# Performance work log

Hardware: AMD Instinct MI355X
Metric: run time of the kernel (lower is better)

Reference implementation:

```python
import jax, jax.numpy as jnp
import numpy as np

B, T, DIN, D = 8, 2048, 1024, 1024
EPS = 1e-6


def setup_inputs() -> dict:
    key = jax.random.key(0)
    k0, k1, k2, k3 = jax.random.split(key, 4)
    x = jax.random.normal(k0, (B, T, DIN), dtype=jnp.float32)
    h0 = jax.random.normal(k1, (B, D), dtype=jnp.float32)
    s0 = jax.random.normal(k2, (B, D), dtype=jnp.float32)
    # xavier_uniform for weight [7D, DIN]
    bound = float(np.sqrt(6.0 / (DIN + 7 * D)))
    W = jax.random.uniform(k3, (7 * D, DIN), dtype=jnp.float32, minval=-bound, maxval=bound)
    # structured bias init from _init_weights: [0, 1, 0, 0, 0, 2, 0.5] per block
    b = jnp.concatenate([
        jnp.zeros(D), jnp.ones(D), jnp.zeros(D), jnp.zeros(D),
        jnp.zeros(D), jnp.full((D,), 2.0), jnp.full((D,), 0.5)
    ]).astype(jnp.float32)
    return {"x": x, "h0": h0, "s0": s0, "W": W, "b": b}


def _forward(x, h0, s0, W, b):
    Bv, Tv, _ = x.shape
    Dv = W.shape[0] // 7
    gates = (jnp.einsum('bti,oi->bto', x, W) + b).reshape(Bv, Tv, 7, Dv)
    r, z, k, v, h_pre, decay, alpha = (gates[:, :, i] for i in range(7))
    # per-element pairwise RMS norms, exactly as in the Triton kernel
    rms_control = jnp.sqrt((r * r + z * z) / 2 + EPS)
    rms_kv = jnp.sqrt((k * k + v * v) / 2 + EPS)
    # r is normalized+sigmoided in the kernel but never used -> no effect on output
    z = jax.nn.sigmoid(z / rms_control)
    decay = jax.nn.sigmoid(decay / jnp.sqrt(decay * decay + EPS))
    alpha = jax.nn.sigmoid(alpha / jnp.sqrt(alpha * alpha + EPS))
    h_pre = h_pre / jnp.sqrt(h_pre * h_pre + EPS)
    kv = (k / rms_kv) * (v / rms_kv) / (rms_kv * rms_kv + EPS)
    # time-major [T,B,D] for the scan
    seq = tuple(jnp.swapaxes(a, 0, 1) for a in (z, kv, h_pre, decay, alpha))

    def step(carry, ins):
        h, s = carry
        z_t, kv_t, hp_t, d_t, a_t = ins
        s = d_t * s + a_t * kv_t
        c = jax.nn.sigmoid(2.0 * (hp_t + s)) * 2.0 - 1.0
        h = (1.0 - z_t) * c + z_t * h
        return (h, s), h

    (_, sT), out = jax.lax.scan(step, (h0, s0), seq)
    return jnp.swapaxes(out, 0, 1), sT  # ([B,T,D], [B,D])


def reference(x, h0, s0, W, b):
    return _forward(x, h0, s0, W, b)
```

## Files before the change

kernel.cpp:

```cpp
#include <hip/hip_runtime.h>
#include <hip/hip_bf16.h>

typedef _Float16 f16x8 __attribute__((ext_vector_type(8)));
typedef float f32x4 __attribute__((ext_vector_type(4)));

static constexpr int BB = 8;
static constexpr int TT = 2048;
static constexpr int DD = 1024;
static constexpr int MM = BB * TT;
static constexpr int NN = 7 * DD;
static constexpr int KP = 3072;
static constexpr int NCSUB = 32;
static constexpr int LC = TT / NCSUB;
static constexpr int BD = BB * DD;
#define EPS_ 1e-6f

static constexpr size_t SZ_CMP = (size_t)MM * DD * 8;
static constexpr size_t SZ_BP  = (size_t)NN * KP * 2;
static constexpr size_t SZ_SM  = (size_t)NCSUB * BD * 4;
static constexpr size_t OFF_BP  = SZ_CMP;
static constexpr size_t OFF_SM  = OFF_BP + SZ_BP;
static constexpr size_t OFF_AP  = OFF_SM + 6 * SZ_SM;
static constexpr size_t CHUNK_BYTES = (size_t)MM * KP * 2 + (size_t)MM * NN * 2;

__device__ __forceinline__ unsigned short bf_rne(float f) {
    unsigned u = __builtin_bit_cast(unsigned, f);
    unsigned r = (u + 0x7fffu + ((u >> 16) & 1u)) >> 16;
    return (unsigned short)r;
}
__device__ __forceinline__ float bf2f(unsigned short u) {
    return __builtin_bit_cast(float, ((unsigned)u) << 16);
}
__device__ __forceinline__ float f16f(unsigned short u) {
    return (float)__builtin_bit_cast(_Float16, u);
}
__device__ __forceinline__ unsigned short f16b(float f) {
    return __builtin_bit_cast(unsigned short, (_Float16)f);
}
__device__ __forceinline__ float sigm(float x) { return 1.0f / (1.0f + __expf(-x)); }

typedef __attribute__((address_space(3))) void lds_void;
typedef const __attribute__((address_space(1))) void gbl_void;
__device__ __forceinline__ void gload16(const void* g, void* l) {
    __builtin_amdgcn_global_load_lds((gbl_void*)g, (lds_void*)l, 16, 0, 0);
}

__global__ __launch_bounds__(256) void prep_w(const float* __restrict__ W,
                                              _Float16* __restrict__ Bp1,
                                              _Float16* __restrict__ Bp2) {
    int i = blockIdx.x * 256 + threadIdx.x;
    int o = i >> 10, k = i & 1023;
    int g = o >> 10, d = o & 1023;
    float wv = W[i] * 512.0f;
    _Float16 w1 = (_Float16)wv;
    _Float16 w2 = (_Float16)(wv - (float)w1);
    if (g == 0 || g == 1 || g == 4) {
        int r1 = (g == 4 ? 2 : g) * 1024 + d;
        Bp1[(size_t)r1 * 1024 + k] = w1;
    } else {
        int r2 = (g < 4 ? g - 2 : g - 3) * 1024 + d;
        size_t base = (size_t)r2 * 3072 + k;
        Bp2[base] = w1; Bp2[base + 1024] = w1; Bp2[base + 2048] = w2;
    }
}

__global__ __launch_bounds__(256) void prep_x(const float* __restrict__ x,
                                              _Float16* __restrict__ Ap,
                                              int tc, int Tc, int tcShift) {
    int i = blockIdx.x * 256 + threadIdx.x;
    int rho = i >> 10, k = i & 1023;
    int b = rho >> tcShift, tau = rho & (Tc - 1);
    size_t m = (size_t)b * TT + (size_t)tc * Tc + tau;
    float xv = x[m * DD + k] * 16.0f;
    _Float16 x1 = (_Float16)xv;
    _Float16 x2 = (_Float16)(xv - (float)x1);
    size_t base = (size_t)rho * KP + k;
    Ap[base] = x1; Ap[base + 1024] = x2; Ap[base + 2048] = x1;
}

template<int KT, int NTILES, int NCOLS, int KIND>
__global__ __launch_bounds__(512) void gemm_k(const _Float16* __restrict__ Ap,
                                              const _Float16* __restrict__ Bp,
                                              const float* __restrict__ bias,
                                              _Float16* __restrict__ Gc, int Mt) {
    constexpr int KSTR = KT * 64;
    __shared__ __align__(16) _Float16 As[256 * 64];
    __shared__ __align__(16) _Float16 Bs[128 * 64];
    int nwg = Mt * NTILES;
    int bid = blockIdx.x;
    int cpx = nwg >> 3;
    int swz = (bid & 7) * cpx + (bid >> 3);
    int bm = swz / NTILES, bn = swz % NTILES;
    int m0 = bm * 256, n0 = bn * 128;
    int tid = threadIdx.x;
    int w = tid >> 6, l = tid & 63;
    int wm = w >> 1, wn = w & 1;
    int lrow = l & 15, kg = l >> 4;
    f32x4 acc[4][4] = {};
    const char* Ab = (const char*)Ap;
    const char* Bb = (const char*)Bp;
    for (int k0 = 0; k0 < KT * 64; k0 += 64) {
#pragma unroll
        for (int q = 0; q < 4; ++q) {
            int c = q * 512 + tid;
            int row = c >> 3, sgg = (c & 7) ^ (row & 7);
            gload16(Ab + ((size_t)(m0 + row) * KP + k0 + sgg * 8) * 2, (char*)As + c * 16);
        }
#pragma unroll
        for (int q = 0; q < 2; ++q) {
            int c = q * 512 + tid;
            int row = c >> 3, sgg = (c & 7) ^ (row & 7);
            gload16(Bb + ((size_t)(n0 + row) * KSTR + k0 + sgg * 8) * 2, (char*)Bs + c * 16);
        }
        __syncthreads();
#pragma unroll
        for (int kk = 0; kk < 64; kk += 32) {
            f16x8 af[4], bfr[4];
            int sgb = kg + (kk >> 3);
#pragma unroll
            for (int i = 0; i < 4; ++i) {
                int r = wm * 64 + i * 16 + lrow;
                af[i] = *(const f16x8*)(As + r * 64 + (size_t)((sgb ^ (r & 7)) * 8));
            }
#pragma unroll
            for (int j = 0; j < 4; ++j) {
                int r = wn * 64 + j * 16 + lrow;
                bfr[j] = *(const f16x8*)(Bs + r * 64 + (size_t)((sgb ^ (r & 7)) * 8));
            }
#pragma unroll
            for (int i = 0; i < 4; ++i)
#pragma unroll
                for (int j = 0; j < 4; ++j)
                    acc[i][j] = __builtin_amdgcn_mfma_f32_16x16x32_f16(af[i], bfr[j], acc[i][j], 0, 0, 0);
        }
        __syncthreads();
    }
    const float inv = 1.0f / 8192.0f;
#pragma unroll
    for (int j = 0; j < 4; ++j) {
        int o = n0 + wn * 64 + j * 16 + lrow;
        int g = o >> 10, d = o & 1023;
        float bv;
        if (KIND == 1) bv = bias[(g == 2 ? 4 : g) * 1024 + d];
        else           bv = bias[(g < 2 ? g + 2 : g + 3) * 1024 + d];
#pragma unroll
        for (int i = 0; i < 4; ++i) {
            int rb = m0 + wm * 64 + i * 16 + kg * 4;
#pragma unroll
            for (int r = 0; r < 4; ++r) {
                float val = acc[i][j][r] * inv + bv;
                if (KIND == 1) {
                    if (g == 2) val = val * rsqrtf(val * val + EPS_);
                } else {
                    if (g >= 2) val = sigm(val * rsqrtf(val * val + EPS_));
                }
                Gc[(size_t)(rb + r) * NCOLS + o] = (_Float16)val;
            }
        }
    }
}

__global__ __launch_bounds__(256) void compact_k(const _Float16* __restrict__ Gc1,
                                                 const _Float16* __restrict__ Gc2,
                                                 ushort4* __restrict__ cmp,
                                                 int tc, int Tc, int tcShift) {
    int idx = blockIdx.x * 256 + threadIdx.x;
    int rho = idx >> 10, d = idx & 1023;
    const _Float16* row1 = Gc1 + (size_t)rho * 3072;
    const _Float16* row2 = Gc2 + (size_t)rho * 4096;
    float r   = row1[d], z  = row1[1024 + d], hpn = row1[2048 + d];
    float k   = row2[d], v  = row2[1024 + d];
    float ds  = row2[2048 + d], as = row2[3072 + d];
    float rc2 = (r * r + z * z) * 0.5f + EPS_;
    float zs = sigm(z * rsqrtf(rc2));
    float rk2 = (k * k + v * v) * 0.5f + EPS_;
    float kv = (k * v) / (rk2 * (rk2 + EPS_));
    float akv = as * kv;
    int b = rho >> tcShift, tau = rho & (Tc - 1);
    size_t m = (size_t)b * TT + (size_t)tc * Tc + tau;
    ushort4 u;
    u.x = bf_rne(akv); u.y = f16b(ds); u.z = f16b(zs); u.w = f16b(hpn);
    cmp[m * DD + d] = u;
}

__global__ __launch_bounds__(256) void passA(const ushort4* __restrict__ cmp,
                                             float* __restrict__ SP, float* __restrict__ SQ) {
    int bid = blockIdx.x;
    int b = bid >> 7, rem = bid & 127;
    int ch = rem >> 2, d = (rem & 3) * 256 + threadIdx.x;
    const ushort4* p = cmp + ((size_t)(b * TT + ch * LC)) * DD + d;
    float P = 1.0f, Q = 0.0f;
#pragma unroll 4
    for (int i = 0; i < LC; ++i) {
        ushort4 u = p[(size_t)i * DD];
        float akv = bf2f(u.x), ds = f16f(u.y);
        P *= ds; Q = ds * Q + akv;
    }
    int bd = b * DD + d;
    SP[ch * BD + bd] = P; SQ[ch * BD + bd] = Q;
}

__global__ __launch_bounds__(256) void passB(const float* __restrict__ s0,
                                             const float* __restrict__ SP, const float* __restrict__ SQ,
                                             float* __restrict__ Sst, float* __restrict__ sT) {
    int bd = blockIdx.x * 256 + threadIdx.x;
    float s = s0[bd];
    for (int ch = 0; ch < NCSUB; ++ch) {
        Sst[ch * BD + bd] = s;
        s = SP[ch * BD + bd] * s + SQ[ch * BD + bd];
    }
    sT[bd] = s;
}

__global__ __launch_bounds__(256) void passC(const ushort4* __restrict__ cmp,
                                             const float* __restrict__ Sst,
                                             float* __restrict__ HZ, float* __restrict__ HR) {
    int bid = blockIdx.x;
    int b = bid >> 7, rem = bid & 127;
    int ch = rem >> 2, d = (rem & 3) * 256 + threadIdx.x;
    int bd = b * DD + d;
    float s = Sst[ch * BD + bd];
    float Z = 1.0f, R = 0.0f;
    const ushort4* p = cmp + ((size_t)(b * TT + ch * LC)) * DD + d;
#pragma unroll 4
    for (int i = 0; i < LC; ++i) {
        ushort4 u = p[(size_t)i * DD];
        float akv = bf2f(u.x), ds = f16f(u.y), zs = f16f(u.z), hpn = f16f(u.w);
        s = ds * s + akv;
        float c = 2.0f * sigm(2.0f * (hpn + s)) - 1.0f;
        Z *= zs; R = zs * R + (1.0f - zs) * c;
    }
    HZ[ch * BD + bd] = Z; HR[ch * BD + bd] = R;
}

__global__ __launch_bounds__(256) void passD(const float* __restrict__ h0,
                                             const float* __restrict__ HZ, const float* __restrict__ HR,
                                             float* __restrict__ Hst) {
    int bd = blockIdx.x * 256 + threadIdx.x;
    float h = h0[bd];
    for (int ch = 0; ch < NCSUB; ++ch) {
        Hst[ch * BD + bd] = h;
        h = HZ[ch * BD + bd] * h + HR[ch * BD + bd];
    }
}

__global__ __launch_bounds__(256) void passE(const ushort4* __restrict__ cmp,
                                             const float* __restrict__ Sst,
                                             const float* __restrict__ Hst,
                                             float* __restrict__ out) {
    int bid = blockIdx.x;
    int b = bid >> 7, rem = bid & 127;
    int ch = rem >> 2, d = (rem & 3) * 256 + threadIdx.x;
    int bd = b * DD + d;
    float s = Sst[ch * BD + bd];
    float h = Hst[ch * BD + bd];
    const ushort4* p = cmp + ((size_t)(b * TT + ch * LC)) * DD + d;
    float* op = out + ((size_t)(b * TT + ch * LC)) * DD + d;
#pragma unroll 4
    for (int i = 0; i < LC; ++i) {
        ushort4 u = p[(size_t)i * DD];
        float akv = bf2f(u.x), ds = f16f(u.y), zs = f16f(u.z), hpn = f16f(u.w);
        s = ds * s + akv;
        float c = 2.0f * sigm(2.0f * (hpn + s)) - 1.0f;
        h = (1.0f - zs) * c + zs * h;
        op[(size_t)i * DD] = h;
    }
}

__global__ __launch_bounds__(256) void sentinel_k(float* __restrict__ sT) {
    int i = blockIdx.x * 256 + threadIdx.x;
    if (i < BD) sT[i] = 1e9f;
}

extern "C" void kernel_launch(void* const* d_in, const int* in_sizes, int n_in,
                              void* d_out, int out_size, void* d_ws, size_t ws_size,
                              hipStream_t stream) {
    const float* x    = (const float*)d_in[0];
    const float* h0   = (const float*)d_in[1];
    const float* s0   = (const float*)d_in[2];
    const float* W    = (const float*)d_in[3];
    const float* bias = (const float*)d_in[4];
    float* out = (float*)d_out;
    float* sT  = out + (size_t)MM * DD;
    char* ws = (char*)d_ws;

    int NCH = 0;
    for (int c : {4, 8, 16, 32}) {
        if (OFF_AP + CHUNK_BYTES / c <= ws_size) { NCH = c; break; }
    }
    if (!NCH) {
        sentinel_k<<<BD / 256, 256, 0, stream>>>(sT);
        return;
    }
    int Mc = MM / NCH;
    int Tc = TT / NCH;
    int tcShift = 31 - __builtin_clz(Tc);
    int Mt = Mc / 256;

    ushort4* cmp = (ushort4*)ws;
    _Float16* Bp1 = (_Float16*)(ws + OFF_BP);
    _Float16* Bp2 = (_Float16*)(ws + OFF_BP + (size_t)3072 * 1024 * 2);
    float* SP  = (float*)(ws + OFF_SM);
    float* SQ  = (float*)(ws + OFF_SM + 1 * SZ_SM);
    float* Sst = (float*)(ws + OFF_SM + 2 * SZ_SM);
    float* HZ  = (float*)(ws + OFF_SM + 3 * SZ_SM);
    float* HR  = (float*)(ws + OFF_SM + 4 * SZ_SM);
    float* Hst = (float*)(ws + OFF_SM + 5 * SZ_SM);
    _Float16* Ap  = (_Float16*)(ws + OFF_AP);
    _Float16* Gc1 = (_Float16*)(ws + OFF_AP + (size_t)Mc * KP * 2);
    _Float16* Gc2 = Gc1 + (size_t)Mc * 3072;

    prep_w<<<(NN * DD) / 256, 256, 0, stream>>>(W, Bp1, Bp2);
    for (int tc = 0; tc < NCH; ++tc) {
        prep_x<<<Mc * 4, 256, 0, stream>>>(x, Ap, tc, Tc, tcShift);
        gemm_k<16, 24, 3072, 1><<<Mt * 24, 512, 0, stream>>>(Ap, Bp1, bias, Gc1, Mt);
        gemm_k<48, 32, 4096, 2><<<Mt * 32, 512, 0, stream>>>(Ap, Bp2, bias, Gc2, Mt);
        compact_k<<<Mc * 4, 256, 0, stream>>>(Gc1, Gc2, cmp, tc, Tc, tcShift);
    }
    passA<<<BB * NCSUB * 4, 256, 0, stream>>>(cmp, SP, SQ);
    passB<<<BD / 256, 256, 0, stream>>>(s0, SP, SQ, Sst, sT);
    passC<<<BB * NCSUB * 4, 256, 0, stream>>>(cmp, Sst, HZ, HR);
    passD<<<BD / 256, 256, 0, stream>>>(h0, HZ, HR, Hst);
    passE<<<BB * NCSUB * 4, 256, 0, stream>>>(cmp, Sst, Hst, out);
}
```

Before: 763.0 us.

## Shrink split-fp16 activation buffer, split compact stream, allow fewer GEMM chunks

The prep kernel now writes only the two fp16 halves of x (hi, lo) instead of a redundant third copy, and the GEMM wraps its K index with a mask so the third K segment rereads the hi half. The per-step compact record is split into two ushort2 arrays, so passA, which needs only akv and decay, reads half the bytes. The smaller chunk footprint lets the launcher try two time chunks, cutting kernel launches and giving larger GEMM grids. Passes C and E now issue two loads per step instead of one.

```diff
diff --git a/kernel.cpp b/kernel.cpp
--- a/kernel.cpp
+++ b/kernel.cpp
@@ -9,19 +9,19 @@
 static constexpr int DD = 1024;
 static constexpr int MM = BB * TT;
 static constexpr int NN = 7 * DD;
-static constexpr int KP = 3072;
+static constexpr int APS = 2048;
 static constexpr int NCSUB = 32;
 static constexpr int LC = TT / NCSUB;
 static constexpr int BD = BB * DD;
 #define EPS_ 1e-6f
 
 static constexpr size_t SZ_CMP = (size_t)MM * DD * 8;
-static constexpr size_t SZ_BP  = (size_t)NN * KP * 2;
+static constexpr size_t SZ_BP  = (size_t)NN * 3072 * 2;
 static constexpr size_t SZ_SM  = (size_t)NCSUB * BD * 4;
 static constexpr size_t OFF_BP  = SZ_CMP;
 static constexpr size_t OFF_SM  = OFF_BP + SZ_BP;
 static constexpr size_t OFF_AP  = OFF_SM + 6 * SZ_SM;
-static constexpr size_t CHUNK_BYTES = (size_t)MM * KP * 2 + (size_t)MM * NN * 2;
+static constexpr size_t CHUNK_BYTES = (size_t)MM * 18432;
 
 __device__ __forceinline__ unsigned short bf_rne(float f) {
     unsigned u = __builtin_bit_cast(unsigned, f);
@@ -74,8 +74,8 @@
     float xv = x[m * DD + k] * 16.0f;
     _Float16 x1 = (_Float16)xv;
     _Float16 x2 = (_Float16)(xv - (float)x1);
-    size_t base = (size_t)rho * KP + k;
-    Ap[base] = x1; Ap[base + 1024] = x2; Ap[base + 2048] = x1;
+    size_t base = (size_t)rho * APS + k;
+    Ap[base] = x1; Ap[base + 1024] = x2;
 }
 
 template<int KT, int NTILES, int NCOLS, int KIND>
@@ -100,11 +100,12 @@
     const char* Ab = (const char*)Ap;
     const char* Bb = (const char*)Bp;
     for (int k0 = 0; k0 < KT * 64; k0 += 64) {
+        int ak0 = k0 & 2047;
 #pragma unroll
         for (int q = 0; q < 4; ++q) {
             int c = q * 512 + tid;
             int row = c >> 3, sgg = (c & 7) ^ (row & 7);
-            gload16(Ab + ((size_t)(m0 + row) * KP + k0 + sgg * 8) * 2, (char*)As + c * 16);
+            gload16(Ab + ((size_t)(m0 + row) * APS + ak0 + sgg * 8) * 2, (char*)As + c * 16);
         }
 #pragma unroll
         for (int q = 0; q < 2; ++q) {
@@ -162,7 +163,8 @@
 
 __global__ __launch_bounds__(256) void compact_k(const _Float16* __restrict__ Gc1,
                                                  const _Float16* __restrict__ Gc2,
-                                                 ushort4* __restrict__ cmp,
+                                                 ushort2* __restrict__ cmpA,
+                                                 ushort2* __restrict__ cmpB,
                                                  int tc, int Tc, int tcShift) {
     int idx = blockIdx.x * 256 + threadIdx.x;
     int rho = idx >> 10, d = idx & 1023;
@@ -178,21 +180,22 @@
     float akv = as * kv;
     int b = rho >> tcShift, tau = rho & (Tc - 1);
     size_t m = (size_t)b * TT + (size_t)tc * Tc + tau;
-    ushort4 u;
-    u.x = bf_rne(akv); u.y = f16b(ds); u.z = f16b(zs); u.w = f16b(hpn);
-    cmp[m * DD + d] = u;
-}
-
-__global__ __launch_bounds__(256) void passA(const ushort4* __restrict__ cmp,
+    ushort2 ua; ua.x = bf_rne(akv); ua.y = f16b(ds);
+    ushort2 ub; ub.x = f16b(zs);    ub.y = f16b(hpn);
+    cmpA[m * DD + d] = ua;
+    cmpB[m * DD + d] = ub;
+}
+
+__global__ __launch_bounds__(256) void passA(const ushort2* __restrict__ cmpA,
                                              float* __restrict__ SP, float* __restrict__ SQ) {
     int bid = blockIdx.x;
     int b = bid >> 7, rem = bid & 127;
     int ch = rem >> 2, d = (rem & 3) * 256 + threadIdx.x;
-    const ushort4* p = cmp + ((size_t)(b * TT + ch * LC)) * DD + d;
+    const ushort2* p = cmpA + ((size_t)(b * TT + ch * LC)) * DD + d;
     float P = 1.0f, Q = 0.0f;
 #pragma unroll 4
     for (int i = 0; i < LC; ++i) {
-        ushort4 u = p[(size_t)i * DD];
+        ushort2 u = p[(size_t)i * DD];
         float akv = bf2f(u.x), ds = f16f(u.y);
         P *= ds; Q = ds * Q + akv;
     }
@@ -212,7 +215,8 @@
     sT[bd] = s;
 }
 
-__global__ __launch_bounds__(256) void passC(const ushort4* __restrict__ cmp,
+__global__ __launch_bounds__(256) void passC(const ushort2* __restrict__ cmpA,
+                                             const ushort2* __restrict__ cmpB,
                                              const float* __restrict__ Sst,
                                              float* __restrict__ HZ, float* __restrict__ HR) {
     int bid = blockIdx.x;
@@ -221,11 +225,12 @@
     int bd = b * DD + d;
     float s = Sst[ch * BD + bd];
     float Z = 1.0f, R = 0.0f;
-    const ushort4* p = cmp + ((size_t)(b * TT + ch * LC)) * DD + d;
+    size_t base = ((size_t)(b * TT + ch * LC)) * DD + d;
 #pragma unroll 4
     for (int i = 0; i < LC; ++i) {
-        ushort4 u = p[(size_t)i * DD];
-        float akv = bf2f(u.x), ds = f16f(u.y), zs = f16f(u.z), hpn = f16f(u.w);
+        ushort2 ua = cmpA[base + (size_t)i * DD];
+        ushort2 ub = cmpB[base + (size_t)i * DD];
+        float akv = bf2f(ua.x), ds = f16f(ua.y), zs = f16f(ub.x), hpn = f16f(ub.y);
         s = ds * s + akv;
         float c = 2.0f * sigm(2.0f * (hpn + s)) - 1.0f;
         Z *= zs; R = zs * R + (1.0f - zs) * c;
@@ -244,7 +249,8 @@
     }
 }
 
-__global__ __launch_bounds__(256) void passE(const ushort4* __restrict__ cmp,
+__global__ __launch_bounds__(256) void passE(const ushort2* __restrict__ cmpA,
+                                             const ushort2* __restrict__ cmpB,
                                              const float* __restrict__ Sst,
                                              const float* __restrict__ Hst,
                                              float* __restrict__ out) {
@@ -254,12 +260,13 @@
     int bd = b * DD + d;
     float s = Sst[ch * BD + bd];
     float h = Hst[ch * BD + bd];
-    const ushort4* p = cmp + ((size_t)(b * TT + ch * LC)) * DD + d;
-    float* op = out + ((size_t)(b * TT + ch * LC)) * DD + d;
+    size_t base = ((size_t)(b * TT + ch * LC)) * DD + d;
+    float* op = out + base;
 #pragma unroll 4
     for (int i = 0; i < LC; ++i) {
-        ushort4 u = p[(size_t)i * DD];
-        float akv = bf2f(u.x), ds = f16f(u.y), zs = f16f(u.z), hpn = f16f(u.w);
+        ushort2 ua = cmpA[base + (size_t)i * DD];
+        ushort2 ub = cmpB[base + (size_t)i * DD];
+        float akv = bf2f(ua.x), ds = f16f(ua.y), zs = f16f(ub.x), hpn = f16f(ub.y);
         s = ds * s + akv;
         float c = 2.0f * sigm(2.0f * (hpn + s)) - 1.0f;
         h = (1.0f - zs) * c + zs * h;
@@ -285,7 +292,7 @@
     char* ws = (char*)d_ws;
 
     int NCH = 0;
-    for (int c : {4, 8, 16, 32}) {
+    for (int c : {2, 4, 8, 16, 32}) {
         if (OFF_AP + CHUNK_BYTES / c <= ws_size) { NCH = c; break; }
     }
     if (!NCH) {
@@ -297,7 +304,8 @@
     int tcShift = 31 - __builtin_clz(Tc);
     int Mt = Mc / 256;
 
-    ushort4* cmp = (ushort4*)ws;
+    ushort2* cmpA = (ushort2*)ws;
+    ushort2* cmpB = (ushort2*)(ws + (size_t)MM * DD * 4);
     _Float16* Bp1 = (_Float16*)(ws + OFF_BP);
     _Float16* Bp2 = (_Float16*)(ws + OFF_BP + (size_t)3072 * 1024 * 2);
     float* SP  = (float*)(ws + OFF_SM);
@@ -307,7 +315,7 @@
     float* HR  = (float*)(ws + OFF_SM + 4 * SZ_SM);
     float* Hst = (float*)(ws + OFF_SM + 5 * SZ_SM);
     _Float16* Ap  = (_Float16*)(ws + OFF_AP);
-    _Float16* Gc1 = (_Float16*)(ws + OFF_AP + (size_t)Mc * KP * 2);
+    _Float16* Gc1 = (_Float16*)(ws + OFF_AP + (size_t)Mc * APS * 2);
     _Float16* Gc2 = Gc1 + (size_t)Mc * 3072;
 
     prep_w<<<(NN * DD) / 256, 256, 0, stream>>>(W, Bp1, Bp2);
@@ -315,11 +323,11 @@
         prep_x<<<Mc * 4, 256, 0, stream>>>(x, Ap, tc, Tc, tcShift);
         gemm_k<16, 24, 3072, 1><<<Mt * 24, 512, 0, stream>>>(Ap, Bp1, bias, Gc1, Mt);
         gemm_k<48, 32, 4096, 2><<<Mt * 32, 512, 0, stream>>>(Ap, Bp2, bias, Gc2, Mt);
-        compact_k<<<Mc * 4, 256, 0, stream>>>(Gc1, Gc2, cmp, tc, Tc, tcShift);
-    }
-    passA<<<BB * NCSUB * 4, 256, 0, stream>>>(cmp, SP, SQ);
+        compact_k<<<Mc * 4, 256, 0, stream>>>(Gc1, Gc2, cmpA, cmpB, tc, Tc, tcShift);
+    }
+    passA<<<BB * NCSUB * 4, 256, 0, stream>>>(cmpA, SP, SQ);
     passB<<<BD / 256, 256, 0, stream>>>(s0, SP, SQ, Sst, sT);
-    passC<<<BB * NCSUB * 4, 256, 0, stream>>>(cmp, Sst, HZ, HR);
+    passC<<<BB * NCSUB * 4, 256, 0, stream>>>(cmpA, cmpB, Sst, HZ, HR);
     passD<<<BD / 256, 256, 0, stream>>>(h0, HZ, HR, Hst);
-    passE<<<BB * NCSUB * 4, 256, 0, stream>>>(cmp, Sst, Hst, out);
-}
+    passE<<<BB * NCSUB * 4, 256, 0, stream>>>(cmpA, cmpB, Sst, Hst, out);
+}
```

After: 754.7 us (median of 2 runs). Within noise of the previous version (-1.1%).
